# Optimization experiments

Hardware: AMD Instinct MI355X
Metric: run time of the kernel (lower is better)

## Reference

```python
import math
import jax, jax.numpy as jnp
import numpy as np

# Frozen random shifts from the original module's __init__ (random.randint(-1,1))
SHIFT_C = 1   # p_2_0_1: roll along channel dim
SHIFT_H = 1   # p_4_1_0: roll along h
SHIFT_W = -1  # p_4_1_1: roll along w
K = 7         # horizontal window size (F.unfold kernel (1,7), padding (0,3))


def setup_inputs() -> dict:
    key = jax.random.key(0)
    k1, k2 = jax.random.split(key)
    n, c, h, w = 8, 256, 56, 56
    x = jax.random.normal(k1, (n, c, h, w), dtype=jnp.float32)
    # p_1_w ~ trunc_normal(std=0.1) around 1.0; approximate with 1 + 0.1*normal
    p1w = 1.0 + 0.1 * jax.random.normal(k2, (1, c, h, w), dtype=jnp.float32)
    return {"x": x, "p1w": p1w}


def _unfold_w7(t):
    # t: (n,c,h,w) -> (n,c,7,h,w): 7 horizontal taps, zero-padded (pad=3)
    w = t.shape[-1]
    tp = jnp.pad(t, ((0, 0), (0, 0), (0, 0), (3, 3)))
    return jnp.stack([tp[..., j:j + w] for j in range(K)], axis=2)


def reference(x, p1w):
    n, c, h, w = x.shape
    hw = h * w
    t1 = p1w * x                              # (n,c,h,w)
    t2 = jnp.roll(t1, SHIFT_C, axis=1)        # roll channels
    t3 = _unfold_w7(t2)                       # (n,c,7,h,w)
    t4 = jnp.roll(jnp.roll(t3, SHIFT_H, axis=3), SHIFT_W, axis=4)
    t5 = t1[:, :, None] - t3                  # (n,c,7,h,w)
    t6 = x[:, :, None] + t4                   # (n,c,7,h,w)
    x2 = x.reshape(n, c, hw)
    t5r = t5.reshape(n, c, K, hw)
    t6r = t6.reshape(n, c, K, hw)
    # scores: bmm(x (n,c,hw), t5^T (n,hw,c*7)) -> (n,c,c,7)
    t7 = jnp.einsum('nip,njkp->nijk', x2, t5r) / math.sqrt(hw)
    # aggregate: bmm(t7 (n,c,c*7), t6 (n,c*7,hw)) -> (n,c,hw)
    t8 = jnp.einsum('nijk,njkp->nip', t7, t6r) / math.sqrt(c * K)
    return t8.reshape(n, c, h, w)
```

## Files before the change

### kernel.cpp

```cpp
#include <hip/hip_runtime.h>

typedef unsigned short u16;
typedef __bf16 bf16x8 __attribute__((ext_vector_type(8)));
typedef float f32x4 __attribute__((ext_vector_type(4)));

#define HH  56
#define WW  56
#define HW  3136
#define CC  256
#define NB  8
#define CKP 2048
#define KS1 4

__device__ __forceinline__ u16 f2bf(float f) {
  unsigned int u = __float_as_uint(f);
  u += 0x7fffu + ((u >> 16) & 1u);
  return (u16)(u >> 16);
}
__device__ __forceinline__ float bf2f(u16 v) {
  return __uint_as_float((unsigned)v << 16);
}

__device__ __forceinline__ void lds_load16(const void* g, void* l) {
  __builtin_amdgcn_global_load_lds(
      (const __attribute__((address_space(1))) void*)g,
      (__attribute__((address_space(3))) void*)l, 16, 0, 0);
}

__global__ void pass1(const float* __restrict__ x, const float* __restrict__ p1w,
                      u16* __restrict__ t1b, u16* __restrict__ xb) {
  int i = blockIdx.x * 256 + threadIdx.x;
  int cw = i % (CC * HW / 4);
  float4 xv = ((const float4*)x)[i];
  float4 wv = ((const float4*)p1w)[cw];
  uint2 xo = make_uint2((unsigned)f2bf(xv.x) | ((unsigned)f2bf(xv.y) << 16),
                        (unsigned)f2bf(xv.z) | ((unsigned)f2bf(xv.w) << 16));
  ((uint2*)xb)[i] = xo;
  uint2 to = make_uint2((unsigned)f2bf(xv.x * wv.x) | ((unsigned)f2bf(xv.y * wv.y) << 16),
                        (unsigned)f2bf(xv.z * wv.z) | ((unsigned)f2bf(xv.w * wv.w) << 16));
  ((uint2*)t1b)[i] = to;
}

__global__ __launch_bounds__(256)
void gemm1f(const u16* __restrict__ A, const u16* __restrict__ t1b,
            float* __restrict__ Cp) {
  __shared__ u16 As[128 * 64];
  __shared__ u16 Bs[128 * 64];

  const int z = blockIdx.z, nb = z / KS1, ks = z % KS1;
  const int it0 = 49 * ks / KS1, it1 = 49 * (ks + 1) / KS1;
  const u16* Ab  = A   + (long)nb * CC * HW;
  const u16* t1n = t1b + (long)nb * CC * HW;
  const int m0 = blockIdx.x * 128, n0 = blockIdx.y * 128;
  const int jb = blockIdx.y * 16;
  const int t = threadIdx.x;
  const int lane = t & 63, wave = t >> 6;
  const int wm = wave & 1, wn = wave >> 1;
  const int lm = lane & 15, quad = lane >> 4;

  const int jl = (t >> 3) & 15, pc = t & 7, hf = t >> 7;
  const int j  = jb + jl;
  const int jm = (j + CC - 1) & (CC - 1);
  const u16* arow = t1n + (long)j  * HW;
  const u16* wrow = t1n + (long)jm * HW;

  f32x4 acc[4][4];
#pragma unroll
  for (int a = 0; a < 4; ++a)
#pragma unroll
    for (int b = 0; b < 4; ++b) acc[a][b] = (f32x4)0.0f;

  int rowc[4], colc[4];
#pragma unroll
  for (int ci = 0; ci < 4; ++ci) {
    int c = t + ci * 256;
    rowc[ci] = c >> 3;
    colc[ci] = ((c & 7) ^ (rowc[ci] & 7)) * 8;
  }

  for (int it = it0; it < it1; ++it) {
    const int k0 = it * 64;
#pragma unroll
    for (int ci = 0; ci < 4; ++ci)
      lds_load16(Ab + (long)(m0 + rowc[ci]) * HW + k0 + colc[ci],
                 &As[(t + ci * 256) * 8]);

    {
      const int p8 = k0 + pc * 8;
      u16 Ar[8], Wd[24];
      *(uint4*)Ar = *(const uint4*)&arow[p8];
#pragma unroll
      for (int L = 0; L < 3; ++L) {
        int ad = p8 - 8 + L * 8;
        ad = ad < 0 ? 0 : (ad > HW - 8 ? HW - 8 : ad);
        *(uint4*)&Wd[L * 8] = *(const uint4*)&wrow[ad];
      }
      int w0t = p8 % 56;
      float Af[8];
#pragma unroll
      for (int e = 0; e < 8; ++e) Af[e] = bf2f(Ar[e]);
      if (hf == 0) {
#pragma unroll
        for (int k = 0; k < 4; ++k) {
          __attribute__((aligned(16))) __bf16 v[8];
#pragma unroll
          for (int e = 0; e < 8; ++e) {
            int w = w0t + e; if (w >= 56) w -= 56;
            float tap = ((unsigned)(w + k - 3) < 56u) ? bf2f(Wd[e + k + 5]) : 0.f;
            v[e] = (__bf16)(Af[e] - tap);
          }
          *(uint4*)&Bs[(jl * 8 + k) * 64 + (pc ^ k) * 8] = *(const uint4*)v;
        }
      } else {
#pragma unroll
        for (int k = 4; k < 7; ++k) {
          __attribute__((aligned(16))) __bf16 v[8];
#pragma unroll
          for (int e = 0; e < 8; ++e) {
            int w = w0t + e; if (w >= 56) w -= 56;
            float tap = ((unsigned)(w + k - 3) < 56u) ? bf2f(Wd[e + k + 5]) : 0.f;
            v[e] = (__bf16)(Af[e] - tap);
          }
          *(uint4*)&Bs[(jl * 8 + k) * 64 + (pc ^ k) * 8] = *(const uint4*)v;
        }
        *(uint4*)&Bs[(jl * 8 + 7) * 64 + (pc ^ 7) * 8] = make_uint4(0, 0, 0, 0);
      }
    }
    __syncthreads();
#pragma unroll
    for (int kk = 0; kk < 2; ++kk) {
      const int phys = ((kk * 4 + quad) ^ (lm & 7)) * 8;
      bf16x8 af[4], bv[4];
#pragma unroll
      for (int mi = 0; mi < 4; ++mi)
        af[mi] = *(const bf16x8*)&As[(wm * 64 + mi * 16 + lm) * 64 + phys];
#pragma unroll
      for (int ni = 0; ni < 4; ++ni)
        bv[ni] = *(const bf16x8*)&Bs[(wn * 64 + ni * 16 + lm) * 64 + phys];
#pragma unroll
      for (int mi = 0; mi < 4; ++mi)
#pragma unroll
        for (int ni = 0; ni < 4; ++ni)
          acc[mi][ni] = __builtin_amdgcn_mfma_f32_16x16x32_bf16(
              af[mi], bv[ni], acc[mi][ni], 0, 0, 0);
    }
    __syncthreads();
  }

  float* Cb = Cp + ((long)ks * NB + nb) * (long)CC * CKP;
#pragma unroll
  for (int mi = 0; mi < 4; ++mi)
#pragma unroll
    for (int ni = 0; ni < 4; ++ni) {
      int rb = m0 + wm * 64 + mi * 16 + quad * 4;
      int cg = n0 + wn * 64 + ni * 16 + lm;
#pragma unroll
      for (int r = 0; r < 4; ++r)
        Cb[(long)(rb + r) * CKP + cg] = acc[mi][ni][r];
    }
}

__global__ void reduce1(const float* __restrict__ p1, u16* __restrict__ t7) {
  const int i = blockIdx.x * 256 + threadIdx.x;
  const long S = (long)NB * CC * CKP / 4;
  float4 a = ((const float4*)p1)[i];
  float4 b = ((const float4*)p1)[i + S];
  float4 c = ((const float4*)p1)[i + 2 * S];
  float4 d = ((const float4*)p1)[i + 3 * S];
  const float s = 1.0f / 56.0f;
  float e0 = (a.x + b.x + c.x + d.x) * s;
  float e1 = (a.y + b.y + c.y + d.y) * s;
  float e2 = (a.z + b.z + c.z + d.z) * s;
  float e3 = (a.w + b.w + c.w + d.w) * s;
  u16 w3 = (i & 1) ? (u16)0 : f2bf(e3);
  ushort4 o = make_ushort4(f2bf(e0), f2bf(e1), f2bf(e2), w3);
  ((ushort4*)t7)[i] = o;
}

__global__ __launch_bounds__(256)
void gemm2f(const u16* __restrict__ A, const u16* __restrict__ xb,
            const u16* __restrict__ t1b, float* __restrict__ out) {
  __shared__ u16 As[128 * 64];
  __shared__ u16 Bs[64 * 64];

  const int nb = blockIdx.z;
  const u16* Ab  = A   + (long)nb * CC * CKP;
  const u16* xbn = xb  + (long)nb * CC * HW;
  const u16* t1n = t1b + (long)nb * CC * HW;
  const int m0 = blockIdx.x * 128, n0 = blockIdx.y * 64;
  const int t = threadIdx.x;
  const int lane = t & 63, wave = t >> 6;
  const int wm = wave & 1, wn = wave >> 1;
  const int lm = lane & 15, quad = lane >> 4;

  const int pr = t & 63, jg = t >> 6;
  const int p  = n0 + pr;
  const int h  = p / WW, w = p - h * WW;
  const int h2 = (h + HH - 1) % HH;
  const int w2 = (w + 1) % WW;
  const int swz = pr & 7;

  f32x4 acc[4][2];
#pragma unroll
  for (int a = 0; a < 4; ++a)
#pragma unroll
    for (int b = 0; b < 2; ++b) acc[a][b] = (f32x4)0.0f;

  int rowc[4], colc[4];
#pragma unroll
  for (int ci = 0; ci < 4; ++ci) {
    int c = t + ci * 256;
    rowc[ci] = c >> 3;
    colc[ci] = ((c & 7) ^ (rowc[ci] & 7)) * 8;
  }

  for (int it = 0; it < 32; ++it) {
    const int k0 = it * 64;
#pragma unroll
    for (int ci = 0; ci < 4; ++ci)
      lds_load16(Ab + (long)(m0 + rowc[ci]) * CKP + k0 + colc[ci],
                 &As[(t + ci * 256) * 8]);

#pragma unroll
    for (int jj = 0; jj < 2; ++jj) {
      const int jch = it * 8 + jg * 2 + jj;
      const int jmm = (jch + CC - 1) & (CC - 1);
      const float xv = bf2f(xbn[(long)jch * HW + p]);
      const u16* trow = t1n + (long)jmm * HW + h2 * WW;
      __attribute__((aligned(16))) __bf16 v[8];
#pragma unroll
      for (int k = 0; k < 7; ++k) {
        int ww = w2 + k - 3;
        int wc = ww < 0 ? 0 : (ww > 55 ? 55 : ww);
        float tv = bf2f(trow[wc]);
        float tap = ((unsigned)ww < 56u) ? tv : 0.f;
        v[k] = (__bf16)(xv + tap);
      }
      v[7] = (__bf16)0.0f;
      *(uint4*)&Bs[pr * 64 + (((jg * 2 + jj) ^ swz) * 8)] = *(const uint4*)v;
    }
    __syncthreads();
#pragma unroll
    for (int kk = 0; kk < 2; ++kk) {
      const int phys = ((kk * 4 + quad) ^ (lm & 7)) * 8;
      bf16x8 af[4], bv[2];
#pragma unroll
      for (int mi = 0; mi < 4; ++mi)
        af[mi] = *(const bf16x8*)&As[(wm * 64 + mi * 16 + lm) * 64 + phys];
#pragma unroll
      for (int ni = 0; ni < 2; ++ni)
        bv[ni] = *(const bf16x8*)&Bs[(wn * 32 + ni * 16 + lm) * 64 + phys];
#pragma unroll
      for (int mi = 0; mi < 4; ++mi)
#pragma unroll
        for (int ni = 0; ni < 2; ++ni)
          acc[mi][ni] = __builtin_amdgcn_mfma_f32_16x16x32_bf16(
              af[mi], bv[ni], acc[mi][ni], 0, 0, 0);
    }
    __syncthreads();
  }

  const float s2 = 0.023622783f;
  float* Ob = out + (long)nb * CC * HW;
#pragma unroll
  for (int mi = 0; mi < 4; ++mi)
#pragma unroll
    for (int ni = 0; ni < 2; ++ni) {
      int rb = m0 + wm * 64 + mi * 16 + quad * 4;
      int cg = n0 + wn * 32 + ni * 16 + lm;
#pragma unroll
      for (int r = 0; r < 4; ++r)
        Ob[(long)(rb + r) * HW + cg] = acc[mi][ni][r] * s2;
    }
}

extern "C" void kernel_launch(void* const* d_in, const int* in_sizes, int n_in,
                              void* d_out, int out_size, void* d_ws, size_t ws_size,
                              hipStream_t stream) {
  const float* x   = (const float*)d_in[0];
  const float* p1w = (const float*)d_in[1];

  char* ws = (char*)d_ws;
  size_t o = 0;
  u16* xb  = (u16*)(ws + o); o += (size_t)NB * CC * HW * 2;
  u16* t1b = (u16*)(ws + o); o += (size_t)NB * CC * HW * 2;
  u16* t7  = (u16*)(ws + o); o += (size_t)NB * CC * CKP * 2;
  float* p1 = (float*)(ws + o); o += (size_t)KS1 * NB * CC * CKP * 4;

  pass1<<<NB * CC * HW / 4 / 256, 256, 0, stream>>>(x, p1w, t1b, xb);
  gemm1f<<<dim3(2, 16, NB * KS1), 256, 0, stream>>>(xb, t1b, p1);
  reduce1<<<NB * CC * CKP / 4 / 256, 256, 0, stream>>>(p1, t7);
  gemm2f<<<dim3(2, 49, NB), 256, 0, stream>>>(t7, xb, t1b, (float*)d_out);
}
```

Before: 206.0 us.

## Factor subtraction and addition out of GEMM operands via extra k=7 column

Instead of forming t1-tap in gemm1's B operand, the kernel stores raw taps in slots 0-6 and the t1 row itself in slot 7. The reduce step then reconstructs each score as (G - a[k]) scaled, where G is the slot-7 dot product, and writes the row sum into slot 7 of t7. gemm2 likewise loads raw taps plus x in slot 7, so the x term is added through that extra column. This removes the per-element float conversions and arithmetic from operand staging. gemm2 also prefetches the next iteration's tap values into registers across the barrier, and reduce1 now handles 8 outputs per thread. The risk is precision: the subtraction now happens after bf16 rounding and accumulation, which can cause cancellation error.

```diff
diff --git a/kernel.cpp b/kernel.cpp
--- a/kernel.cpp
+++ b/kernel.cpp
@@ -87,7 +87,8 @@
 
     {
       const int p8 = k0 + pc * 8;
-      u16 Ar[8], Wd[24];
+      __attribute__((aligned(16))) u16 Ar[8];
+      __attribute__((aligned(16))) u16 Wd[24];
       *(uint4*)Ar = *(const uint4*)&arow[p8];
 #pragma unroll
       for (int L = 0; L < 3; ++L) {
@@ -95,35 +96,29 @@
         ad = ad < 0 ? 0 : (ad > HW - 8 ? HW - 8 : ad);
         *(uint4*)&Wd[L * 8] = *(const uint4*)&wrow[ad];
       }
-      int w0t = p8 % 56;
-      float Af[8];
-#pragma unroll
-      for (int e = 0; e < 8; ++e) Af[e] = bf2f(Ar[e]);
+      const int w0t = p8 % 56;
+      int wv[8];
+#pragma unroll
+      for (int e = 0; e < 8; ++e) { int w = w0t + e; wv[e] = w >= 56 ? w - 56 : w; }
       if (hf == 0) {
 #pragma unroll
         for (int k = 0; k < 4; ++k) {
-          __attribute__((aligned(16))) __bf16 v[8];
-#pragma unroll
-          for (int e = 0; e < 8; ++e) {
-            int w = w0t + e; if (w >= 56) w -= 56;
-            float tap = ((unsigned)(w + k - 3) < 56u) ? bf2f(Wd[e + k + 5]) : 0.f;
-            v[e] = (__bf16)(Af[e] - tap);
-          }
+          __attribute__((aligned(16))) u16 v[8];
+#pragma unroll
+          for (int e = 0; e < 8; ++e)
+            v[e] = ((unsigned)(wv[e] + k - 3) < 56u) ? Wd[e + k + 5] : (u16)0;
           *(uint4*)&Bs[(jl * 8 + k) * 64 + (pc ^ k) * 8] = *(const uint4*)v;
         }
       } else {
 #pragma unroll
         for (int k = 4; k < 7; ++k) {
-          __attribute__((aligned(16))) __bf16 v[8];
-#pragma unroll
-          for (int e = 0; e < 8; ++e) {
-            int w = w0t + e; if (w >= 56) w -= 56;
-            float tap = ((unsigned)(w + k - 3) < 56u) ? bf2f(Wd[e + k + 5]) : 0.f;
-            v[e] = (__bf16)(Af[e] - tap);
-          }
+          __attribute__((aligned(16))) u16 v[8];
+#pragma unroll
+          for (int e = 0; e < 8; ++e)
+            v[e] = ((unsigned)(wv[e] + k - 3) < 56u) ? Wd[e + k + 5] : (u16)0;
           *(uint4*)&Bs[(jl * 8 + k) * 64 + (pc ^ k) * 8] = *(const uint4*)v;
         }
-        *(uint4*)&Bs[(jl * 8 + 7) * 64 + (pc ^ 7) * 8] = make_uint4(0, 0, 0, 0);
+        *(uint4*)&Bs[(jl * 8 + 7) * 64 + (pc ^ 7) * 8] = *(const uint4*)Ar;
       }
     }
     __syncthreads();
@@ -161,20 +156,31 @@
 }
 
 __global__ void reduce1(const float* __restrict__ p1, u16* __restrict__ t7) {
-  const int i = blockIdx.x * 256 + threadIdx.x;
-  const long S = (long)NB * CC * CKP / 4;
-  float4 a = ((const float4*)p1)[i];
-  float4 b = ((const float4*)p1)[i + S];
-  float4 c = ((const float4*)p1)[i + 2 * S];
-  float4 d = ((const float4*)p1)[i + 3 * S];
+  const int g = blockIdx.x * 256 + threadIdx.x;
+  const long S = (long)NB * CC * CKP;
+  const long base = (long)g * 8;
+  float a[8];
+#pragma unroll
+  for (int e = 0; e < 8; ++e) a[e] = 0.0f;
+#pragma unroll
+  for (int ks = 0; ks < KS1; ++ks) {
+    float4 lo = *(const float4*)&p1[ks * S + base];
+    float4 hi = *(const float4*)&p1[ks * S + base + 4];
+    a[0] += lo.x; a[1] += lo.y; a[2] += lo.z; a[3] += lo.w;
+    a[4] += hi.x; a[5] += hi.y; a[6] += hi.z; a[7] += hi.w;
+  }
   const float s = 1.0f / 56.0f;
-  float e0 = (a.x + b.x + c.x + d.x) * s;
-  float e1 = (a.y + b.y + c.y + d.y) * s;
-  float e2 = (a.z + b.z + c.z + d.z) * s;
-  float e3 = (a.w + b.w + c.w + d.w) * s;
-  u16 w3 = (i & 1) ? (u16)0 : f2bf(e3);
-  ushort4 o = make_ushort4(f2bf(e0), f2bf(e1), f2bf(e2), w3);
-  ((ushort4*)t7)[i] = o;
+  const float G = a[7];
+  __attribute__((aligned(16))) u16 o[8];
+  float s7 = 0.0f;
+#pragma unroll
+  for (int k = 0; k < 7; ++k) {
+    float v = (G - a[k]) * s;
+    s7 += v;
+    o[k] = f2bf(v);
+  }
+  o[7] = f2bf(s7);
+  *(uint4*)&t7[base] = *(const uint4*)o;
 }
 
 __global__ __launch_bounds__(256)
@@ -200,6 +206,15 @@
   const int w2 = (w + 1) % WW;
   const int swz = pr & 7;
 
+  int toff[7], tmsk[7];
+#pragma unroll
+  for (int k = 0; k < 7; ++k) {
+    int ww = w2 + k - 3;
+    int wc = ww < 0 ? 0 : (ww > 55 ? 55 : ww);
+    toff[k] = h2 * WW + wc;
+    tmsk[k] = ((unsigned)ww < 56u);
+  }
+
   f32x4 acc[4][2];
 #pragma unroll
   for (int a = 0; a < 4; ++a)
@@ -214,6 +229,17 @@
     colc[ci] = ((c & 7) ^ (rowc[ci] & 7)) * 8;
   }
 
+  u16 tr[2][7], xr[2];
+#pragma unroll
+  for (int jj = 0; jj < 2; ++jj) {
+    const int jch = jg * 2 + jj;
+    const int jmm = (jch + CC - 1) & (CC - 1);
+    const u16* trow = t1n + (long)jmm * HW;
+#pragma unroll
+    for (int k = 0; k < 7; ++k) tr[jj][k] = trow[toff[k]];
+    xr[jj] = xbn[(long)jch * HW + p];
+  }
+
   for (int it = 0; it < 32; ++it) {
     const int k0 = it * 64;
 #pragma unroll
@@ -223,23 +249,26 @@
 
 #pragma unroll
     for (int jj = 0; jj < 2; ++jj) {
-      const int jch = it * 8 + jg * 2 + jj;
-      const int jmm = (jch + CC - 1) & (CC - 1);
-      const float xv = bf2f(xbn[(long)jch * HW + p]);
-      const u16* trow = t1n + (long)jmm * HW + h2 * WW;
-      __attribute__((aligned(16))) __bf16 v[8];
-#pragma unroll
-      for (int k = 0; k < 7; ++k) {
-        int ww = w2 + k - 3;
-        int wc = ww < 0 ? 0 : (ww > 55 ? 55 : ww);
-        float tv = bf2f(trow[wc]);
-        float tap = ((unsigned)ww < 56u) ? tv : 0.f;
-        v[k] = (__bf16)(xv + tap);
+      __attribute__((aligned(16))) u16 v[8];
+#pragma unroll
+      for (int k = 0; k < 7; ++k) v[k] = tmsk[k] ? tr[jj][k] : (u16)0;
+      v[7] = xr[jj];
+      *(uint4*)&Bs[pr * 64 + (((jg * 2 + jj) ^ swz) * 8)] = *(const uint4*)v;
+    }
+    __syncthreads();
+
+    if (it < 31) {
+#pragma unroll
+      for (int jj = 0; jj < 2; ++jj) {
+        const int jch = (it + 1) * 8 + jg * 2 + jj;
+        const int jmm = (jch + CC - 1) & (CC - 1);
+        const u16* trow = t1n + (long)jmm * HW;
+#pragma unroll
+        for (int k = 0; k < 7; ++k) tr[jj][k] = trow[toff[k]];
+        xr[jj] = xbn[(long)jch * HW + p];
       }
-      v[7] = (__bf16)0.0f;
-      *(uint4*)&Bs[pr * 64 + (((jg * 2 + jj) ^ swz) * 8)] = *(const uint4*)v;
-    }
-    __syncthreads();
+    }
+
 #pragma unroll
     for (int kk = 0; kk < 2; ++kk) {
       const int phys = ((kk * 4 + quad) ^ (lm & 7)) * 8;
@@ -289,6 +318,6 @@
 
   pass1<<<NB * CC * HW / 4 / 256, 256, 0, stream>>>(x, p1w, t1b, xb);
   gemm1f<<<dim3(2, 16, NB * KS1), 256, 0, stream>>>(xb, t1b, p1);
-  reduce1<<<NB * CC * CKP / 4 / 256, 256, 0, stream>>>(p1, t7);
+  reduce1<<<NB * CC * CKP / 8 / 256, 256, 0, stream>>>(p1, t7);
   gemm2f<<<dim3(2, 49, NB), 256, 0, stream>>>(t7, xb, t1b, (float*)d_out);
 }
```

New measurement: 210.8 us. +2.3%, slower.
